# Kernel tuning notes

Hardware: AMD Instinct MI355X
Metric: run time of the kernel (lower is better)

The kernel has to match this reference:

```python
import jax, jax.numpy as jnp
import numpy as np

N = 8192      # num nodes
E = 8192      # num hyperedges
D = 256       # embedding dim
DENSITY = 0.01
LEAKY = 0.2   # negative_slope of LeakyReLU


def setup_inputs() -> dict:
    key = jax.random.key(0)
    k1, k2, k3, k4, k5 = jax.random.split(key, 5)
    # sparse adjacency matrices represented densely (values * bernoulli mask)
    inp_adj = jax.random.normal(k1, (E, N), dtype=jnp.float32) * (
        jax.random.uniform(k2, (E, N)) < DENSITY
    ).astype(jnp.float32)
    att_adj = jax.random.normal(k3, (N, E), dtype=jnp.float32) * (
        jax.random.uniform(k4, (N, E)) < DENSITY
    ).astype(jnp.float32)
    embs = jax.random.normal(k5, (N, D), dtype=jnp.float32)
    return {"inp_adj": inp_adj, "att_adj": att_adj, "embs": embs}


def reference(inp_adj, att_adj, embs):
    # adj = att_adj @ inp_adj  (spgemm in the original)  -> [N, N]
    adj = att_adj @ inp_adj
    # adj @ (adj.T @ embs)  (two spmm)  -> [N, D]
    out = adj @ (adj.T @ embs)
    # LeakyReLU(negative_slope=LEAKY)
    return jnp.where(out > 0, out, LEAKY * out)
```

## Files before the change

kernel.cpp:

```cpp
#include <hip/hip_runtime.h>
#include <stdint.h>

#define NROWS 8192
#define NCOLS 8192
#define DDIM  256
#define SLOTS 160
#define CAP   786432
#define HB    128
#define RPB   (NROWS / HB)

__device__ __forceinline__ float bf16lo(uint32_t u) { return __uint_as_float(u << 16); }
__device__ __forceinline__ float bf16hi(uint32_t u) { return __uint_as_float(u & 0xffff0000u); }
__device__ __forceinline__ uint32_t f2bf(float f) {
    uint32_t b = __float_as_uint(f);
    return (b + 0x7fffu + ((b >> 16) & 1u)) >> 16;
}

__global__ __launch_bounds__(256) void cvt_kernel(const float* __restrict__ in,
                                                  uint32_t* __restrict__ out) {
    int i = blockIdx.x * 256 + threadIdx.x;
    float2 f = ((const float2*)in)[i];
    out[i] = f2bf(f.x) | (f2bf(f.y) << 16);
}

__global__ __launch_bounds__(256) void extract_kernel(
        const float* __restrict__ MA, const float* __restrict__ MB,
        int* __restrict__ rcA, uint2* __restrict__ pairA,
        int* __restrict__ rcB, uint2* __restrict__ pairB) {
    const int wv   = threadIdx.x >> 6;
    const int lane = threadIdx.x & 63;
    const int W = blockIdx.x * 4 + wv;
    const int which = W >> 13;
    const int r = W & (NROWS - 1);
    const float* __restrict__ M = which ? MB : MA;
    int*   rc     = which ? rcB : rcA;
    uint2* g_pair = which ? pairB : pairA;

    const float4* __restrict__ M4 = (const float4*)(M + (size_t)r * NCOLS);
    uint2* __restrict__ dst = g_pair + (size_t)r * SLOTS;
    int base = 0;
    #pragma unroll
    for (int ch = 0; ch < 4; ++ch) {
        float4 d[8];
        #pragma unroll
        for (int i = 0; i < 8; ++i) d[i] = M4[ch * 512 + i * 64 + lane];
        int cnt = 0;
        #pragma unroll
        for (int i = 0; i < 8; ++i)
            cnt += (d[i].x != 0.f) + (d[i].y != 0.f) + (d[i].z != 0.f) + (d[i].w != 0.f);
        int inc = cnt;
        #pragma unroll
        for (int sd = 1; sd < 64; sd <<= 1) {
            int t = __shfl_up(inc, sd, 64);
            if (lane >= sd) inc += t;
        }
        int off = base + inc - cnt;
        int tot = __shfl(inc, 63);
        #pragma unroll
        for (int i = 0; i < 8; ++i) {
            const uint32_t cbase = (uint32_t)((ch * 512 + i * 64 + lane) * 4);
            if (d[i].x != 0.f) { if (off < SLOTS) dst[off] = make_uint2(cbase + 0, __float_as_uint(d[i].x)); ++off; }
            if (d[i].y != 0.f) { if (off < SLOTS) dst[off] = make_uint2(cbase + 1, __float_as_uint(d[i].y)); ++off; }
            if (d[i].z != 0.f) { if (off < SLOTS) dst[off] = make_uint2(cbase + 2, __float_as_uint(d[i].z)); ++off; }
            if (d[i].w != 0.f) { if (off < SLOTS) dst[off] = make_uint2(cbase + 3, __float_as_uint(d[i].w)); ++off; }
        }
        base += tot;
    }
    if (lane == 0) rc[r] = base < SLOTS ? base : SLOTS;
}

__global__ __launch_bounds__(256) void hist_kernel(
        const int* __restrict__ rcA, const uint2* __restrict__ pairA, int* __restrict__ PA,
        const int* __restrict__ rcB, const uint2* __restrict__ pairB, int* __restrict__ PB) {
    const int which = blockIdx.x >> 7;
    const int b = blockIdx.x & (HB - 1);
    const int* rc      = which ? rcB : rcA;
    const uint2* pair  = which ? pairB : pairA;
    int* P = which ? PB : PA;
    __shared__ int h[NCOLS];
    const int tid = threadIdx.x;
    const int wv = tid >> 6, lane = tid & 63;
    for (int i = tid; i < NCOLS; i += 256) h[i] = 0;
    __syncthreads();
    for (int r = b * RPB + wv; r < (b + 1) * RPB; r += 4) {
        const int c = rc[r];
        const uint2* __restrict__ p = pair + (size_t)r * SLOTS;
        for (int j = lane; j < c; j += 64) atomicAdd(&h[p[j].x], 1);
    }
    __syncthreads();
    for (int i = tid; i < NCOLS; i += 256) P[b * NCOLS + i] = h[i];
}

__global__ __launch_bounds__(256) void coltot_kernel(
        const int* __restrict__ PA, int* __restrict__ totA,
        const int* __restrict__ PB, int* __restrict__ totB) {
    const int which = blockIdx.x >> 5;
    const int cb = blockIdx.x & 31;
    const int* P = which ? PB : PA;
    int* tot = which ? totB : totA;
    const int c = cb * 256 + threadIdx.x;
    int sum = 0;
    #pragma unroll 8
    for (int b = 0; b < HB; ++b) sum += P[b * NCOLS + c];
    tot[c] = sum;
}

__global__ __launch_bounds__(256) void prefix_kernel(
        const int* __restrict__ totA, int* __restrict__ startA,
        const int* __restrict__ totB, int* __restrict__ startB) {
    const int* cnt = blockIdx.x ? totB : totA;
    int* start     = blockIdx.x ? startB : startA;
    __shared__ int wtot[4];
    const int tid = threadIdx.x;
    const int wv = tid >> 6, lane = tid & 63;
    const int chunk = NCOLS / 256;
    const int base = tid * chunk;
    int sum = 0;
    for (int i = 0; i < chunk; ++i) sum += cnt[base + i];
    int inc = sum;
    #pragma unroll
    for (int sd = 1; sd < 64; sd <<= 1) {
        int t = __shfl_up(inc, sd, 64);
        if (lane >= sd) inc += t;
    }
    if (lane == 63) wtot[wv] = inc;
    __syncthreads();
    if (tid == 0) {
        int acc = 0;
        #pragma unroll
        for (int i = 0; i < 4; ++i) { int t = wtot[i]; wtot[i] = acc; acc += t; }
    }
    __syncthreads();
    int run = wtot[wv] + inc - sum;
    for (int i = 0; i < chunk; ++i) { start[base + i] = run; run += cnt[base + i]; }
}

__global__ __launch_bounds__(256) void offsets_kernel(
        int* __restrict__ PA, const int* __restrict__ startA,
        int* __restrict__ PB, const int* __restrict__ startB) {
    const int which = blockIdx.x >> 5;
    const int cb = blockIdx.x & 31;
    int* P = which ? PB : PA;
    const int* start = which ? startB : startA;
    const int c = cb * 256 + threadIdx.x;
    int run = start[c];
    for (int b = 0; b < HB; ++b) {
        int t = P[b * NCOLS + c];
        P[b * NCOLS + c] = run;
        run += t;
    }
}

__global__ __launch_bounds__(256) void scatter_kernel(
        const int* __restrict__ rcA, const uint2* __restrict__ pairA,
        const int* __restrict__ PA, uint2* __restrict__ cscA,
        const int* __restrict__ rcB, const uint2* __restrict__ pairB,
        const int* __restrict__ PB, uint2* __restrict__ cscB) {
    const int which = blockIdx.x >> 7;
    const int b = blockIdx.x & (HB - 1);
    const int* rc     = which ? rcB : rcA;
    const uint2* pair = which ? pairB : pairA;
    const int* P      = which ? PB : PA;
    uint2* csc        = which ? cscB : cscA;
    __shared__ int cur[NCOLS];
    const int tid = threadIdx.x;
    const int wv = tid >> 6, lane = tid & 63;
    for (int i = tid; i < NCOLS; i += 256) cur[i] = P[b * NCOLS + i];
    __syncthreads();
    for (int r = b * RPB + wv; r < (b + 1) * RPB; r += 4) {
        const int c = rc[r];
        const uint2* __restrict__ p = pair + (size_t)r * SLOTS;
        for (int j = lane; j < c; j += 64) {
            uint2 e = p[j];
            int slot = atomicAdd(&cur[e.x], 1);
            csc[slot] = make_uint2((uint32_t)r, e.y);
        }
    }
}

struct Acc8 { float a0, a1, a2, a3, a4, a5, a6, a7; };

__device__ __forceinline__ void fma8(Acc8& a, float v, uint4 t) {
    a.a0 = fmaf(v, bf16lo(t.x), a.a0); a.a1 = fmaf(v, bf16hi(t.x), a.a1);
    a.a2 = fmaf(v, bf16lo(t.y), a.a2); a.a3 = fmaf(v, bf16hi(t.y), a.a3);
    a.a4 = fmaf(v, bf16lo(t.z), a.a4); a.a5 = fmaf(v, bf16hi(t.z), a.a5);
    a.a6 = fmaf(v, bf16lo(t.w), a.a6); a.a7 = fmaf(v, bf16hi(t.w), a.a7);
}

template<int FINAL>
__global__ __launch_bounds__(256) void spmm_kernel(
        const int* __restrict__ start, const int* __restrict__ cnt,
        const uint2* __restrict__ pairs,
        const uint4* __restrict__ X,
        void* __restrict__ Y, int fixed_stride) {
    const int wv   = threadIdx.x >> 6;
    const int lane = threadIdx.x & 63;
    const int half = lane >> 5, sub = lane & 31;
    const int r = blockIdx.x * 4 + wv;
    const int c = cnt[r];
    const uint2* __restrict__ P = pairs + (fixed_stride ? (size_t)r * SLOTS : (size_t)start[r]);
    Acc8 a = {0.f, 0.f, 0.f, 0.f, 0.f, 0.f, 0.f, 0.f};
    int j = 0;
    for (; j + 15 < c; j += 16) {
        uint2 p[8];
        uint4 x[8];
        #pragma unroll
        for (int t = 0; t < 8; ++t) p[t] = P[j + 2 * t + half];
        #pragma unroll
        for (int t = 0; t < 8; ++t) x[t] = X[(size_t)p[t].x * 32 + sub];
        #pragma unroll
        for (int t = 0; t < 8; ++t) fma8(a, __uint_as_float(p[t].y), x[t]);
    }
    for (; j + 1 < c; j += 2) {
        uint2 p = P[j + half];
        uint4 x = X[(size_t)p.x * 32 + sub];
        fma8(a, __uint_as_float(p.y), x);
    }
    if (j < c) {
        uint2 p = P[j];
        uint4 x = X[(size_t)p.x * 32 + sub];
        float v = half ? 0.f : __uint_as_float(p.y);
        fma8(a, v, x);
    }
    a.a0 += __shfl_xor(a.a0, 32); a.a1 += __shfl_xor(a.a1, 32);
    a.a2 += __shfl_xor(a.a2, 32); a.a3 += __shfl_xor(a.a3, 32);
    a.a4 += __shfl_xor(a.a4, 32); a.a5 += __shfl_xor(a.a5, 32);
    a.a6 += __shfl_xor(a.a6, 32); a.a7 += __shfl_xor(a.a7, 32);
    if (half == 0) {
        if (FINAL) {
            a.a0 = a.a0 > 0.f ? a.a0 : 0.2f * a.a0; a.a1 = a.a1 > 0.f ? a.a1 : 0.2f * a.a1;
            a.a2 = a.a2 > 0.f ? a.a2 : 0.2f * a.a2; a.a3 = a.a3 > 0.f ? a.a3 : 0.2f * a.a3;
            a.a4 = a.a4 > 0.f ? a.a4 : 0.2f * a.a4; a.a5 = a.a5 > 0.f ? a.a5 : 0.2f * a.a5;
            a.a6 = a.a6 > 0.f ? a.a6 : 0.2f * a.a6; a.a7 = a.a7 > 0.f ? a.a7 : 0.2f * a.a7;
            float4* Y4 = (float4*)Y;
            Y4[(size_t)r * 64 + sub * 2]     = make_float4(a.a0, a.a1, a.a2, a.a3);
            Y4[(size_t)r * 64 + sub * 2 + 1] = make_float4(a.a4, a.a5, a.a6, a.a7);
        } else {
            uint4 o;
            o.x = f2bf(a.a0) | (f2bf(a.a1) << 16);
            o.y = f2bf(a.a2) | (f2bf(a.a3) << 16);
            o.z = f2bf(a.a4) | (f2bf(a.a5) << 16);
            o.w = f2bf(a.a6) | (f2bf(a.a7) << 16);
            ((uint4*)Y)[(size_t)r * 32 + sub] = o;
        }
    }
}

extern "C" void kernel_launch(void* const* d_in, const int* in_sizes, int n_in,
                              void* d_out, int out_size, void* d_ws, size_t ws_size,
                              hipStream_t stream) {
    const float* Bm   = (const float*)d_in[0];
    const float* Am   = (const float*)d_in[1];
    const float* embs = (const float*)d_in[2];
    float* out = (float*)d_out;

    char* w = (char*)d_ws;
    auto alloc = [&](size_t bytes) -> char* {
        char* p = w;
        w += (bytes + 255) & ~(size_t)255;
        return p;
    };
    uint32_t* embs16 = (uint32_t*)alloc((size_t)NROWS * DDIM * 2);
    uint32_t* t1     = (uint32_t*)alloc((size_t)NROWS * DDIM * 2);
    uint32_t* t2     = (uint32_t*)alloc((size_t)NROWS * DDIM * 2);
    uint32_t* t3     = t1;

    int* rcA       = (int*)alloc(NROWS * 4);
    int* rcB       = (int*)alloc(NROWS * 4);
    int* coltotA   = (int*)alloc(NCOLS * 4);
    int* colstartA = (int*)alloc(NCOLS * 4);
    int* coltotB   = (int*)alloc(NCOLS * 4);
    int* colstartB = (int*)alloc(NCOLS * 4);
    int* PA        = (int*)alloc((size_t)HB * NCOLS * 4);
    int* PB        = (int*)alloc((size_t)HB * NCOLS * 4);

    uint2* csrA = (uint2*)alloc((size_t)NROWS * SLOTS * 8);
    uint2* csrB = (uint2*)alloc((size_t)NROWS * SLOTS * 8);
    uint2* cscA = (uint2*)alloc((size_t)CAP * 8);
    uint2* cscB = (uint2*)alloc((size_t)CAP * 8);

    cvt_kernel<<<(NROWS * DDIM / 2) / 256, 256, 0, stream>>>(embs, embs16);
    extract_kernel<<<2 * NROWS / 4, 256, 0, stream>>>(Am, Bm, rcA, csrA, rcB, csrB);
    hist_kernel<<<2 * HB, 256, 0, stream>>>(rcA, csrA, PA, rcB, csrB, PB);
    coltot_kernel<<<64, 256, 0, stream>>>(PA, coltotA, PB, coltotB);
    prefix_kernel<<<2, 256, 0, stream>>>(coltotA, colstartA, coltotB, colstartB);
    offsets_kernel<<<64, 256, 0, stream>>>(PA, colstartA, PB, colstartB);
    scatter_kernel<<<2 * HB, 256, 0, stream>>>(rcA, csrA, PA, cscA, rcB, csrB, PB, cscB);
    spmm_kernel<0><<<NROWS / 4, 256, 0, stream>>>(colstartA, coltotA, cscA, (const uint4*)embs16, t1, 0);
    spmm_kernel<0><<<NROWS / 4, 256, 0, stream>>>(colstartB, coltotB, cscB, (const uint4*)t1, t2, 0);
    spmm_kernel<0><<<NROWS / 4, 256, 0, stream>>>(nullptr, rcB, csrB, (const uint4*)t2, t3, 1);
    spmm_kernel<1><<<NROWS / 4, 256, 0, stream>>>(nullptr, rcA, csrA, (const uint4*)t3, out, 1);

    (void)in_sizes; (void)n_in; (void)out_size; (void)ws_size;
}
```

Measured before the change: 693.2 us.

## Pack sparse entries into 32-bit index+bf16 words and split SpMM chain into column halves

Sparse entries are now stored as a single 32-bit word holding a 16-bit column index and a bf16 value, replacing the 8-byte index/float pair. This halves the bandwidth of the CSR/CSC index streams and rounds the adjacency values to bf16, which may reduce accuracy. The embedding and intermediate matrices are also split into two 128-column halves, and the four-SpMM chain runs once per half. The goal is a smaller gathered working set (2 MB per half) that fits better in cache, at the cost of reading the sparse structure twice and launching twice as many kernels.

Measured after the change: 717.8 us. 3.5% more time.

```diff
diff --git a/kernel.cpp b/kernel.cpp
--- a/kernel.cpp
+++ b/kernel.cpp
@@ -4,10 +4,12 @@
 #define NROWS 8192
 #define NCOLS 8192
 #define DDIM  256
+#define HCOLS 128
 #define SLOTS 160
 #define CAP   786432
 #define HB    128
 #define RPB   (NROWS / HB)
+#define HTAB  (NROWS * (HCOLS / 2))
 
 __device__ __forceinline__ float bf16lo(uint32_t u) { return __uint_as_float(u << 16); }
 __device__ __forceinline__ float bf16hi(uint32_t u) { return __uint_as_float(u & 0xffff0000u); }
@@ -19,25 +21,28 @@
 __global__ __launch_bounds__(256) void cvt_kernel(const float* __restrict__ in,
                                                   uint32_t* __restrict__ out) {
     int i = blockIdx.x * 256 + threadIdx.x;
-    float2 f = ((const float2*)in)[i];
-    out[i] = f2bf(f.x) | (f2bf(f.y) << 16);
+    int r  = i >> 7;
+    int cp = i & 127;
+    int h  = cp >> 6;
+    float2 f = ((const float2*)in)[(size_t)r * 128 + cp];
+    out[(size_t)h * HTAB + (size_t)r * 64 + (cp & 63)] = f2bf(f.x) | (f2bf(f.y) << 16);
 }
 
 __global__ __launch_bounds__(256) void extract_kernel(
         const float* __restrict__ MA, const float* __restrict__ MB,
-        int* __restrict__ rcA, uint2* __restrict__ pairA,
-        int* __restrict__ rcB, uint2* __restrict__ pairB) {
+        int* __restrict__ rcA, uint32_t* __restrict__ pairA,
+        int* __restrict__ rcB, uint32_t* __restrict__ pairB) {
     const int wv   = threadIdx.x >> 6;
     const int lane = threadIdx.x & 63;
     const int W = blockIdx.x * 4 + wv;
     const int which = W >> 13;
     const int r = W & (NROWS - 1);
     const float* __restrict__ M = which ? MB : MA;
-    int*   rc     = which ? rcB : rcA;
-    uint2* g_pair = which ? pairB : pairA;
+    int*      rc     = which ? rcB : rcA;
+    uint32_t* g_pair = which ? pairB : pairA;
 
     const float4* __restrict__ M4 = (const float4*)(M + (size_t)r * NCOLS);
-    uint2* __restrict__ dst = g_pair + (size_t)r * SLOTS;
+    uint32_t* __restrict__ dst = g_pair + (size_t)r * SLOTS;
     int base = 0;
     #pragma unroll
     for (int ch = 0; ch < 4; ++ch) {
@@ -59,10 +64,10 @@
         #pragma unroll
         for (int i = 0; i < 8; ++i) {
             const uint32_t cbase = (uint32_t)((ch * 512 + i * 64 + lane) * 4);
-            if (d[i].x != 0.f) { if (off < SLOTS) dst[off] = make_uint2(cbase + 0, __float_as_uint(d[i].x)); ++off; }
-            if (d[i].y != 0.f) { if (off < SLOTS) dst[off] = make_uint2(cbase + 1, __float_as_uint(d[i].y)); ++off; }
-            if (d[i].z != 0.f) { if (off < SLOTS) dst[off] = make_uint2(cbase + 2, __float_as_uint(d[i].z)); ++off; }
-            if (d[i].w != 0.f) { if (off < SLOTS) dst[off] = make_uint2(cbase + 3, __float_as_uint(d[i].w)); ++off; }
+            if (d[i].x != 0.f) { if (off < SLOTS) dst[off] = (cbase + 0) | (f2bf(d[i].x) << 16); ++off; }
+            if (d[i].y != 0.f) { if (off < SLOTS) dst[off] = (cbase + 1) | (f2bf(d[i].y) << 16); ++off; }
+            if (d[i].z != 0.f) { if (off < SLOTS) dst[off] = (cbase + 2) | (f2bf(d[i].z) << 16); ++off; }
+            if (d[i].w != 0.f) { if (off < SLOTS) dst[off] = (cbase + 3) | (f2bf(d[i].w) << 16); ++off; }
         }
         base += tot;
     }
@@ -70,12 +75,12 @@
 }
 
 __global__ __launch_bounds__(256) void hist_kernel(
-        const int* __restrict__ rcA, const uint2* __restrict__ pairA, int* __restrict__ PA,
-        const int* __restrict__ rcB, const uint2* __restrict__ pairB, int* __restrict__ PB) {
+        const int* __restrict__ rcA, const uint32_t* __restrict__ pairA, int* __restrict__ PA,
+        const int* __restrict__ rcB, const uint32_t* __restrict__ pairB, int* __restrict__ PB) {
     const int which = blockIdx.x >> 7;
     const int b = blockIdx.x & (HB - 1);
-    const int* rc      = which ? rcB : rcA;
-    const uint2* pair  = which ? pairB : pairA;
+    const int* rc         = which ? rcB : rcA;
+    const uint32_t* pair  = which ? pairB : pairA;
     int* P = which ? PB : PA;
     __shared__ int h[NCOLS];
     const int tid = threadIdx.x;
@@ -84,8 +89,8 @@
     __syncthreads();
     for (int r = b * RPB + wv; r < (b + 1) * RPB; r += 4) {
         const int c = rc[r];
-        const uint2* __restrict__ p = pair + (size_t)r * SLOTS;
-        for (int j = lane; j < c; j += 64) atomicAdd(&h[p[j].x], 1);
+        const uint32_t* __restrict__ p = pair + (size_t)r * SLOTS;
+        for (int j = lane; j < c; j += 64) atomicAdd(&h[p[j] & 0xFFFFu], 1);
     }
     __syncthreads();
     for (int i = tid; i < NCOLS; i += 256) P[b * NCOLS + i] = h[i];
@@ -152,16 +157,16 @@
 }
 
 __global__ __launch_bounds__(256) void scatter_kernel(
-        const int* __restrict__ rcA, const uint2* __restrict__ pairA,
-        const int* __restrict__ PA, uint2* __restrict__ cscA,
-        const int* __restrict__ rcB, const uint2* __restrict__ pairB,
-        const int* __restrict__ PB, uint2* __restrict__ cscB) {
+        const int* __restrict__ rcA, const uint32_t* __restrict__ pairA,
+        const int* __restrict__ PA, uint32_t* __restrict__ cscA,
+        const int* __restrict__ rcB, const uint32_t* __restrict__ pairB,
+        const int* __restrict__ PB, uint32_t* __restrict__ cscB) {
     const int which = blockIdx.x >> 7;
     const int b = blockIdx.x & (HB - 1);
-    const int* rc     = which ? rcB : rcA;
-    const uint2* pair = which ? pairB : pairA;
-    const int* P      = which ? PB : PA;
-    uint2* csc        = which ? cscB : cscA;
+    const int* rc        = which ? rcB : rcA;
+    const uint32_t* pair = which ? pairB : pairA;
+    const int* P         = which ? PB : PA;
+    uint32_t* csc        = which ? cscB : cscA;
     __shared__ int cur[NCOLS];
     const int tid = threadIdx.x;
     const int wv = tid >> 6, lane = tid & 63;
@@ -169,79 +174,71 @@
     __syncthreads();
     for (int r = b * RPB + wv; r < (b + 1) * RPB; r += 4) {
         const int c = rc[r];
-        const uint2* __restrict__ p = pair + (size_t)r * SLOTS;
+        const uint32_t* __restrict__ p = pair + (size_t)r * SLOTS;
         for (int j = lane; j < c; j += 64) {
-            uint2 e = p[j];
-            int slot = atomicAdd(&cur[e.x], 1);
-            csc[slot] = make_uint2((uint32_t)r, e.y);
-        }
-    }
-}
-
-struct Acc8 { float a0, a1, a2, a3, a4, a5, a6, a7; };
-
-__device__ __forceinline__ void fma8(Acc8& a, float v, uint4 t) {
-    a.a0 = fmaf(v, bf16lo(t.x), a.a0); a.a1 = fmaf(v, bf16hi(t.x), a.a1);
-    a.a2 = fmaf(v, bf16lo(t.y), a.a2); a.a3 = fmaf(v, bf16hi(t.y), a.a3);
-    a.a4 = fmaf(v, bf16lo(t.z), a.a4); a.a5 = fmaf(v, bf16hi(t.z), a.a5);
-    a.a6 = fmaf(v, bf16lo(t.w), a.a6); a.a7 = fmaf(v, bf16hi(t.w), a.a7);
+            uint32_t e = p[j];
+            int slot = atomicAdd(&cur[e & 0xFFFFu], 1);
+            csc[slot] = (uint32_t)r | (e & 0xFFFF0000u);
+        }
+    }
 }
 
 template<int FINAL>
 __global__ __launch_bounds__(256) void spmm_kernel(
         const int* __restrict__ start, const int* __restrict__ cnt,
-        const uint2* __restrict__ pairs,
-        const uint4* __restrict__ X,
-        void* __restrict__ Y, int fixed_stride) {
+        const uint32_t* __restrict__ pairs,
+        const uint2* __restrict__ X,
+        void* __restrict__ Y,
+        int fixed_stride) {
     const int wv   = threadIdx.x >> 6;
     const int lane = threadIdx.x & 63;
     const int half = lane >> 5, sub = lane & 31;
     const int r = blockIdx.x * 4 + wv;
     const int c = cnt[r];
-    const uint2* __restrict__ P = pairs + (fixed_stride ? (size_t)r * SLOTS : (size_t)start[r]);
-    Acc8 a = {0.f, 0.f, 0.f, 0.f, 0.f, 0.f, 0.f, 0.f};
+    const uint32_t* __restrict__ P = pairs + (fixed_stride ? (size_t)r * SLOTS : (size_t)start[r]);
+    float a0 = 0.f, a1 = 0.f, a2 = 0.f, a3 = 0.f;
     int j = 0;
     for (; j + 15 < c; j += 16) {
-        uint2 p[8];
-        uint4 x[8];
+        uint32_t p[8];
+        uint2 x[8];
         #pragma unroll
         for (int t = 0; t < 8; ++t) p[t] = P[j + 2 * t + half];
         #pragma unroll
-        for (int t = 0; t < 8; ++t) x[t] = X[(size_t)p[t].x * 32 + sub];
-        #pragma unroll
-        for (int t = 0; t < 8; ++t) fma8(a, __uint_as_float(p[t].y), x[t]);
+        for (int t = 0; t < 8; ++t) x[t] = X[(size_t)(p[t] & 0xFFFFu) * 32 + sub];
+        #pragma unroll
+        for (int t = 0; t < 8; ++t) {
+            float v = __uint_as_float(p[t] & 0xFFFF0000u);
+            a0 = fmaf(v, bf16lo(x[t].x), a0); a1 = fmaf(v, bf16hi(x[t].x), a1);
+            a2 = fmaf(v, bf16lo(x[t].y), a2); a3 = fmaf(v, bf16hi(x[t].y), a3);
+        }
     }
     for (; j + 1 < c; j += 2) {
-        uint2 p = P[j + half];
-        uint4 x = X[(size_t)p.x * 32 + sub];
-        fma8(a, __uint_as_float(p.y), x);
+        uint32_t p = P[j + half];
+        uint2 x = X[(size_t)(p & 0xFFFFu) * 32 + sub];
+        float v = __uint_as_float(p & 0xFFFF0000u);
+        a0 = fmaf(v, bf16lo(x.x), a0); a1 = fmaf(v, bf16hi(x.x), a1);
+        a2 = fmaf(v, bf16lo(x.y), a2); a3 = fmaf(v, bf16hi(x.y), a3);
     }
     if (j < c) {
-        uint2 p = P[j];
-        uint4 x = X[(size_t)p.x * 32 + sub];
-        float v = half ? 0.f : __uint_as_float(p.y);
-        fma8(a, v, x);
-    }
-    a.a0 += __shfl_xor(a.a0, 32); a.a1 += __shfl_xor(a.a1, 32);
-    a.a2 += __shfl_xor(a.a2, 32); a.a3 += __shfl_xor(a.a3, 32);
-    a.a4 += __shfl_xor(a.a4, 32); a.a5 += __shfl_xor(a.a5, 32);
-    a.a6 += __shfl_xor(a.a6, 32); a.a7 += __shfl_xor(a.a7, 32);
+        uint32_t p = P[j];
+        uint2 x = X[(size_t)(p & 0xFFFFu) * 32 + sub];
+        float v = half ? 0.f : __uint_as_float(p & 0xFFFF0000u);
+        a0 = fmaf(v, bf16lo(x.x), a0); a1 = fmaf(v, bf16hi(x.x), a1);
+        a2 = fmaf(v, bf16lo(x.y), a2); a3 = fmaf(v, bf16hi(x.y), a3);
+    }
+    a0 += __shfl_xor(a0, 32); a1 += __shfl_xor(a1, 32);
+    a2 += __shfl_xor(a2, 32); a3 += __shfl_xor(a3, 32);
     if (half == 0) {
         if (FINAL) {
-            a.a0 = a.a0 > 0.f ? a.a0 : 0.2f * a.a0; a.a1 = a.a1 > 0.f ? a.a1 : 0.2f * a.a1;
-            a.a2 = a.a2 > 0.f ? a.a2 : 0.2f * a.a2; a.a3 = a.a3 > 0.f ? a.a3 : 0.2f * a.a3;
-            a.a4 = a.a4 > 0.f ? a.a4 : 0.2f * a.a4; a.a5 = a.a5 > 0.f ? a.a5 : 0.2f * a.a5;
-            a.a6 = a.a6 > 0.f ? a.a6 : 0.2f * a.a6; a.a7 = a.a7 > 0.f ? a.a7 : 0.2f * a.a7;
-            float4* Y4 = (float4*)Y;
-            Y4[(size_t)r * 64 + sub * 2]     = make_float4(a.a0, a.a1, a.a2, a.a3);
-            Y4[(size_t)r * 64 + sub * 2 + 1] = make_float4(a.a4, a.a5, a.a6, a.a7);
+            a0 = a0 > 0.f ? a0 : 0.2f * a0; a1 = a1 > 0.f ? a1 : 0.2f * a1;
+            a2 = a2 > 0.f ? a2 : 0.2f * a2; a3 = a3 > 0.f ? a3 : 0.2f * a3;
+            float* yr = (float*)Y + (size_t)r * DDIM + sub * 4;
+            ((float4*)yr)[0] = make_float4(a0, a1, a2, a3);
         } else {
-            uint4 o;
-            o.x = f2bf(a.a0) | (f2bf(a.a1) << 16);
-            o.y = f2bf(a.a2) | (f2bf(a.a3) << 16);
-            o.z = f2bf(a.a4) | (f2bf(a.a5) << 16);
-            o.w = f2bf(a.a6) | (f2bf(a.a7) << 16);
-            ((uint4*)Y)[(size_t)r * 32 + sub] = o;
+            uint2 o;
+            o.x = f2bf(a0) | (f2bf(a1) << 16);
+            o.y = f2bf(a2) | (f2bf(a3) << 16);
+            ((uint2*)Y)[(size_t)r * 32 + sub] = o;
         }
     }
 }
@@ -260,9 +257,9 @@
         w += (bytes + 255) & ~(size_t)255;
         return p;
     };
-    uint32_t* embs16 = (uint32_t*)alloc((size_t)NROWS * DDIM * 2);
-    uint32_t* t1     = (uint32_t*)alloc((size_t)NROWS * DDIM * 2);
-    uint32_t* t2     = (uint32_t*)alloc((size_t)NROWS * DDIM * 2);
+    uint32_t* embs16 = (uint32_t*)alloc((size_t)2 * HTAB * 4);
+    uint32_t* t1     = (uint32_t*)alloc((size_t)2 * HTAB * 4);
+    uint32_t* t2     = (uint32_t*)alloc((size_t)2 * HTAB * 4);
     uint32_t* t3     = t1;
 
     int* rcA       = (int*)alloc(NROWS * 4);
@@ -274,22 +271,30 @@
     int* PA        = (int*)alloc((size_t)HB * NCOLS * 4);
     int* PB        = (int*)alloc((size_t)HB * NCOLS * 4);
 
-    uint2* csrA = (uint2*)alloc((size_t)NROWS * SLOTS * 8);
-    uint2* csrB = (uint2*)alloc((size_t)NROWS * SLOTS * 8);
-    uint2* cscA = (uint2*)alloc((size_t)CAP * 8);
-    uint2* cscB = (uint2*)alloc((size_t)CAP * 8);
-
-    cvt_kernel<<<(NROWS * DDIM / 2) / 256, 256, 0, stream>>>(embs, embs16);
+    uint32_t* csrA = (uint32_t*)alloc((size_t)NROWS * SLOTS * 4);
+    uint32_t* csrB = (uint32_t*)alloc((size_t)NROWS * SLOTS * 4);
+    uint32_t* cscA = (uint32_t*)alloc((size_t)CAP * 4);
+    uint32_t* cscB = (uint32_t*)alloc((size_t)CAP * 4);
+
+    cvt_kernel<<<(NROWS * 128) / 256, 256, 0, stream>>>(embs, embs16);
     extract_kernel<<<2 * NROWS / 4, 256, 0, stream>>>(Am, Bm, rcA, csrA, rcB, csrB);
     hist_kernel<<<2 * HB, 256, 0, stream>>>(rcA, csrA, PA, rcB, csrB, PB);
     coltot_kernel<<<64, 256, 0, stream>>>(PA, coltotA, PB, coltotB);
     prefix_kernel<<<2, 256, 0, stream>>>(coltotA, colstartA, coltotB, colstartB);
     offsets_kernel<<<64, 256, 0, stream>>>(PA, colstartA, PB, colstartB);
     scatter_kernel<<<2 * HB, 256, 0, stream>>>(rcA, csrA, PA, cscA, rcB, csrB, PB, cscB);
-    spmm_kernel<0><<<NROWS / 4, 256, 0, stream>>>(colstartA, coltotA, cscA, (const uint4*)embs16, t1, 0);
-    spmm_kernel<0><<<NROWS / 4, 256, 0, stream>>>(colstartB, coltotB, cscB, (const uint4*)t1, t2, 0);
-    spmm_kernel<0><<<NROWS / 4, 256, 0, stream>>>(nullptr, rcB, csrB, (const uint4*)t2, t3, 1);
-    spmm_kernel<1><<<NROWS / 4, 256, 0, stream>>>(nullptr, rcA, csrA, (const uint4*)t3, out, 1);
+
+    for (int h = 0; h < 2; ++h) {
+        const uint2* Xe = (const uint2*)(embs16 + (size_t)h * HTAB);
+        uint2* T1 = (uint2*)(t1 + (size_t)h * HTAB);
+        uint2* T2 = (uint2*)(t2 + (size_t)h * HTAB);
+        uint2* T3 = (uint2*)(t3 + (size_t)h * HTAB);
+        spmm_kernel<0><<<NROWS / 4, 256, 0, stream>>>(colstartA, coltotA, cscA, Xe, T1, 0);
+        spmm_kernel<0><<<NROWS / 4, 256, 0, stream>>>(colstartB, coltotB, cscB, (const uint2*)T1, T2, 0);
+        spmm_kernel<0><<<NROWS / 4, 256, 0, stream>>>(nullptr, rcB, csrB, (const uint2*)T2, T3, 1);
+        spmm_kernel<1><<<NROWS / 4, 256, 0, stream>>>(nullptr, rcA, csrA, (const uint2*)T3,
+                                                      out + h * HCOLS, 1);
+    }
 
     (void)in_sizes; (void)n_in; (void)out_size; (void)ws_size;
 }
```
